# Kernel tuning notes

Measured on AMD Instinct MI355X. Metric: run time of the kernel, lower is better.

## Reference

```python
import jax, jax.numpy as jnp
import numpy as np

B, C, T = 32, 64, 8192
OUT, K = 129, 32
TWO_PI = 2.0 * np.pi
DROP_THRESH = 0.1  # squared-distance threshold for channel dropping


def setup_inputs() -> dict:
    key = jax.random.key(0)
    k1, k2, k3, k4, k5 = jax.random.split(key, 5)
    X = jax.random.normal(k1, (B, C, T), dtype=jnp.float32)
    positions = jax.random.uniform(k2, (B, C, 2), dtype=jnp.float32)
    drop_idx = jax.random.randint(k3, (B,), 0, C)
    scale = 1.0 / (K * K)
    z_real = jax.random.normal(k4, (OUT, K * K), dtype=jnp.float32) * scale
    z_imag = jax.random.normal(k5, (OUT, K * K), dtype=jnp.float32) * scale
    return {"X": X, "positions": positions, "drop_idx": drop_idx,
            "z_real": z_real, "z_imag": z_imag}


def reference(X, positions, drop_idx, z_real, z_imag):
    # frequency grid: feature index f = l_idx*K + k_idx (row-major over [l, k])
    kk = jnp.arange(1, K + 1, dtype=jnp.float32)
    coef_k = jnp.tile(kk, K)            # [K*K] varies fastest
    coef_l = jnp.repeat(kk, K)          # [K*K]

    x = positions[..., 0]               # [B, C]
    y = positions[..., 1]
    # phase: [B, C, K*K]
    phase = TWO_PI * (x[..., None] * coef_k + y[..., None] * coef_l)
    cos_mat = jnp.cos(phase)
    sin_mat = jnp.sin(phase)

    # a: [B, OUT, C]
    a = (jnp.einsum('of,bcf->boc', z_real, cos_mat)
         + jnp.einsum('of,bcf->boc', z_imag, sin_mat))

    # channel drop: remove all channels within sqdist < 0.1 of the dropped electrode
    pd = positions[jnp.arange(B), drop_idx]                 # [B, 2]
    dist = jnp.sum((positions - pd[:, None, :]) ** 2, axis=-1)  # [B, C]
    keep = dist >= DROP_THRESH                              # [B, C]

    a = jnp.where(keep[:, None, :], a, -1e9)
    attn = jax.nn.softmax(a, axis=2)                        # [B, OUT, C]
    # out: [B, OUT, T]
    return jnp.einsum('boc,bct->bot', attn, X)
```

## Files before the change

kernel.cpp:

```cpp
#include <hip/hip_runtime.h>
#include <math.h>

typedef __bf16 bf16x8 __attribute__((ext_vector_type(8)));
typedef unsigned short u16x8 __attribute__((ext_vector_type(8)));
typedef float f32x4 __attribute__((ext_vector_type(4)));

namespace {
constexpr int kB   = 32;
constexpr int kC   = 64;
constexpr int kT   = 8192;
constexpr int kOUT = 129;
constexpr int kKK  = 1024;
constexpr int kNKC = 8;
constexpr int kOP  = 144;
}

__device__ inline float sin2pi(float r) {
  float o; asm("v_sin_f32 %0, %1" : "=v"(o) : "v"(r)); return o;
}
__device__ inline float cos2pi(float r) {
  float o; asm("v_cos_f32 %0, %1" : "=v"(o) : "v"(r)); return o;
}
__device__ inline unsigned short f2bf_rne(float f) {
  unsigned int u = __builtin_bit_cast(unsigned int, f);
  return (unsigned short)((u + 0x7fffu + ((u >> 16) & 1u)) >> 16);
}
__device__ inline float bf2f(unsigned short h) {
  return __builtin_bit_cast(float, (unsigned int)h << 16);
}
__device__ inline void split8(const float* v, bf16x8& hi, bf16x8& lo) {
  u16x8 h, l;
#pragma unroll
  for (int j = 0; j < 8; ++j) {
    const unsigned short hh = f2bf_rne(v[j]);
    h[j] = hh;
    l[j] = f2bf_rne(v[j] - bf2f(hh));
  }
  hi = __builtin_bit_cast(bf16x8, h);
  lo = __builtin_bit_cast(bf16x8, l);
}
__device__ inline bf16x8 ldbf8(const unsigned short* p) {
  return __builtin_bit_cast(bf16x8, *reinterpret_cast<const u16x8*>(p));
}

__global__ __launch_bounds__(256) void sa_split_z(
    const float* __restrict__ z_real, const float* __restrict__ z_imag,
    unsigned short* __restrict__ zrh, unsigned short* __restrict__ zrl,
    unsigned short* __restrict__ zih, unsigned short* __restrict__ zil)
{
  const int i = blockIdx.x * 256 + threadIdx.x;
  if (i >= 128 * kOP * 8) return;
  const int fj = i & 7;
  const int o  = (i >> 3) % kOP;
  const int fb = i / (kOP * 8);
  const int f  = fb * 8 + fj;
  float vr = 0.f, vi = 0.f;
  if (o < kOUT) {
    vr = z_real[(size_t)o * kKK + f];
    vi = z_imag[(size_t)o * kKK + f];
  }
  unsigned short h = f2bf_rne(vr);
  zrh[i] = h; zrl[i] = f2bf_rne(vr - bf2f(h));
  h = f2bf_rne(vi);
  zih[i] = h; zil[i] = f2bf_rne(vi - bf2f(h));
}

__global__ __launch_bounds__(256) void sa_cis(
    const float* __restrict__ positions,
    unsigned short* __restrict__ csh, unsigned short* __restrict__ csl,
    unsigned short* __restrict__ snh, unsigned short* __restrict__ snl)
{
  const int i = blockIdx.x * 256 + threadIdx.x;
  const int fj = i & 7;
  const int c  = (i >> 3) & 63;
  const int fb = (i >> 9) & 127;
  const int b  = i >> 16;
  const int f  = fb * 8 + fj;
  const float2 p = reinterpret_cast<const float2*>(positions)[b * kC + c];
  const float kf = (float)((f & 31) + 1);
  const float lf = (float)((f >> 5) + 1);
  const float w = __fadd_rn(__fmul_rn(p.x, kf), __fmul_rn(p.y, lf));
  const float r = w - floorf(w);
  const float cs = cos2pi(r);
  const float sn = sin2pi(r);
  unsigned short h = f2bf_rne(cs);
  csh[i] = h; csl[i] = f2bf_rne(cs - bf2f(h));
  h = f2bf_rne(sn);
  snh[i] = h; snl[i] = f2bf_rne(sn - bf2f(h));
}

__global__ __launch_bounds__(256) void sa_phase_gemm(
    const unsigned short* __restrict__ zrh, const unsigned short* __restrict__ zrl,
    const unsigned short* __restrict__ zih, const unsigned short* __restrict__ zil,
    const unsigned short* __restrict__ csh, const unsigned short* __restrict__ csl,
    const unsigned short* __restrict__ snh, const unsigned short* __restrict__ snl,
    float* __restrict__ part)
{
  const int bid = blockIdx.x;
  const int b   = bid & 31;
  const int kc  = (bid >> 5) & 7;
  const int mh  = bid >> 8;
  const int w    = threadIdx.x >> 6;
  const int lane = threadIdx.x & 63;
  const int cg   = lane >> 4;
  const int cl   = lane & 15;
  const int c    = w * 16 + cl;

  bf16x8 BcH[4], BcL[4], BsH[4], BsL[4];
#pragma unroll
  for (int ks = 0; ks < 4; ++ks) {
    const size_t off = ((size_t)(b * 128 + kc * 16 + ks * 4 + cg) * kC + c) * 8;
    BcH[ks] = ldbf8(csh + off);
    BcL[ks] = ldbf8(csl + off);
    BsH[ks] = ldbf8(snh + off);
    BsL[ks] = ldbf8(snl + off);
  }

  const int nm  = mh ? 4 : 5;
  const int ob0 = mh * 80;

#pragma unroll
  for (int m = 0; m < 5; ++m) {
    if (m < nm) {
      const int ob = ob0 + m * 16;
      const int oa = ob + cl;
      f32x4 acc = {0.f, 0.f, 0.f, 0.f};
#pragma unroll
      for (int ks = 0; ks < 4; ++ks) {
        const size_t zo = ((size_t)(kc * 16 + ks * 4 + cg) * kOP + oa) * 8;
        const bf16x8 ArH = ldbf8(zrh + zo);
        const bf16x8 ArL = ldbf8(zrl + zo);
        const bf16x8 AiH = ldbf8(zih + zo);
        const bf16x8 AiL = ldbf8(zil + zo);
        acc = __builtin_amdgcn_mfma_f32_16x16x32_bf16(ArH, BcH[ks], acc, 0, 0, 0);
        acc = __builtin_amdgcn_mfma_f32_16x16x32_bf16(ArH, BcL[ks], acc, 0, 0, 0);
        acc = __builtin_amdgcn_mfma_f32_16x16x32_bf16(ArL, BcH[ks], acc, 0, 0, 0);
        acc = __builtin_amdgcn_mfma_f32_16x16x32_bf16(AiH, BsH[ks], acc, 0, 0, 0);
        acc = __builtin_amdgcn_mfma_f32_16x16x32_bf16(AiH, BsL[ks], acc, 0, 0, 0);
        acc = __builtin_amdgcn_mfma_f32_16x16x32_bf16(AiL, BsH[ks], acc, 0, 0, 0);
      }
#pragma unroll
      for (int r = 0; r < 4; ++r) {
        const int o = ob + cg * 4 + r;
        if (o < kOUT)
          part[(((size_t)kc * kB + b) * kOUT + o) * kC + c] = acc[r];
      }
    }
  }
}

__global__ __launch_bounds__(256) void sa_softmax(
    const float* __restrict__ part,
    const float* __restrict__ positions,
    const int*   __restrict__ drop_idx,
    unsigned short* __restrict__ a_hi,
    unsigned short* __restrict__ a_lo)
{
  const int bo = blockIdx.x * 4 + (threadIdx.x >> 6);
  if (bo >= kB * kOUT) return;
  const int b = bo / kOUT;
  const int o = bo - b * kOUT;
  const int c = threadIdx.x & 63;

  float a = 0.f;
#pragma unroll
  for (int fc = 0; fc < kNKC; ++fc)
    a += part[(((size_t)fc * kB + b) * kOUT + o) * kC + c];

  const float2 p  = reinterpret_cast<const float2*>(positions)[b * kC + c];
  const int    di = drop_idx[b];
  const float2 pd = reinterpret_cast<const float2*>(positions)[b * kC + di];
  const float dx = p.x - pd.x;
  const float dy = p.y - pd.y;
  const float d2 = __fadd_rn(__fmul_rn(dx, dx), __fmul_rn(dy, dy));
  if (d2 < 0.1f) a = -1e9f;

  float m = a;
#pragma unroll
  for (int off = 32; off; off >>= 1) m = fmaxf(m, __shfl_xor(m, off));
  const float e = expf(a - m);
  float s = e;
#pragma unroll
  for (int off = 32; off; off >>= 1) s += __shfl_xor(s, off);

  const float att = e / s;
  const unsigned short h = f2bf_rne(att);
  a_hi[(size_t)bo * kC + c] = h;
  a_lo[(size_t)bo * kC + c] = f2bf_rne(att - bf2f(h));
}

__global__ __launch_bounds__(256) void sa_apply_mfma(
    const float* __restrict__ X,
    const unsigned short* __restrict__ a_hi,
    const unsigned short* __restrict__ a_lo,
    float* __restrict__ out)
{
  __shared__ unsigned short s_a[2 * 144 * kC];

  const int b   = blockIdx.x >> 5;
  const int tc  = blockIdx.x & 31;
  const int t0  = tc * 256;
  const int tid = threadIdx.x;

  {
    char* sb = reinterpret_cast<char*>(s_a);
    for (int i = tid; i < 2 * 144 * 8; i += 256) {
      const int tile = (i >= 144 * 8) ? 1 : 0;
      const int r    = (i >> 3) - tile * 144;
      const int ch   = i & 7;
      float4 v;
      if (r < kOUT) {
        const unsigned short* src =
            (tile ? a_lo : a_hi) + ((size_t)b * kOUT + r) * kC + ch * 8;
        v = *reinterpret_cast<const float4*>(src);
      } else {
        v = make_float4(0.f, 0.f, 0.f, 0.f);
      }
      const int byte = tile * (144 * 128) + r * 128 + ((ch * 16) ^ ((r & 7) << 4));
      *reinterpret_cast<float4*>(sb + byte) = v;
    }
  }

  const int wave = tid >> 6;
  const int lane = tid & 63;
  const int cl   = lane & 15;
  const int cg   = lane >> 4;
  const int tb   = t0 + wave * 64;

  const float* Xb = X + (size_t)b * kC * kT;
  bf16x8 Xh[4][2], Xl[4][2];
#pragma unroll
  for (int n = 0; n < 4; ++n) {
    const int t = tb + n * 16 + cl;
    float xv[16];
#pragma unroll
    for (int s2 = 0; s2 < 2; ++s2)
#pragma unroll
      for (int j = 0; j < 8; ++j)
        xv[s2 * 8 + j] = Xb[(size_t)(s2 * 32 + cg * 8 + j) * kT + t];
    split8(xv,     Xh[n][0], Xl[n][0]);
    split8(xv + 8, Xh[n][1], Xl[n][1]);
  }

  __syncthreads();

  const char* sb = reinterpret_cast<const char*>(s_a);
  float* outb = out + (size_t)b * kOUT * kT;

  for (int m = 0; m < 9; ++m) {
    const int row  = m * 16 + cl;
    const int base = row * 128;
    const int sw   = (row & 7) << 4;
    const int gb   = cg * 16;

    const bf16x8 Ah0 = *reinterpret_cast<const bf16x8*>(sb + base + ((gb     ) ^ sw));
    const bf16x8 Ah1 = *reinterpret_cast<const bf16x8*>(sb + base + ((gb + 64) ^ sw));
    const bf16x8 Al0 = *reinterpret_cast<const bf16x8*>(sb + 144 * 128 + base + ((gb     ) ^ sw));
    const bf16x8 Al1 = *reinterpret_cast<const bf16x8*>(sb + 144 * 128 + base + ((gb + 64) ^ sw));

    f32x4 acc[4];
#pragma unroll
    for (int n = 0; n < 4; ++n) {
      acc[n] = f32x4{0.f, 0.f, 0.f, 0.f};
      acc[n] = __builtin_amdgcn_mfma_f32_16x16x32_bf16(Ah0, Xh[n][0], acc[n], 0, 0, 0);
      acc[n] = __builtin_amdgcn_mfma_f32_16x16x32_bf16(Ah1, Xh[n][1], acc[n], 0, 0, 0);
      acc[n] = __builtin_amdgcn_mfma_f32_16x16x32_bf16(Al0, Xh[n][0], acc[n], 0, 0, 0);
      acc[n] = __builtin_amdgcn_mfma_f32_16x16x32_bf16(Al1, Xh[n][1], acc[n], 0, 0, 0);
      acc[n] = __builtin_amdgcn_mfma_f32_16x16x32_bf16(Ah0, Xl[n][0], acc[n], 0, 0, 0);
      acc[n] = __builtin_amdgcn_mfma_f32_16x16x32_bf16(Ah1, Xl[n][1], acc[n], 0, 0, 0);
    }

#pragma unroll
    for (int n = 0; n < 4; ++n)
#pragma unroll
      for (int r = 0; r < 4; ++r) {
        const int o = m * 16 + cg * 4 + r;
        if (o < kOUT)
          outb[(size_t)o * kT + tb + n * 16 + cl] = acc[n][r];
      }
  }
}

extern "C" void kernel_launch(void* const* d_in, const int* in_sizes, int n_in,
                              void* d_out, int out_size, void* d_ws, size_t ws_size,
                              hipStream_t stream) {
  (void)in_sizes; (void)n_in; (void)out_size; (void)ws_size;
  const float* X         = (const float*)d_in[0];
  const float* positions = (const float*)d_in[1];
  const int*   drop_idx  = (const int*)d_in[2];
  const float* z_real    = (const float*)d_in[3];
  const float* z_imag    = (const float*)d_in[4];
  float* out = (float*)d_out;

  char* wsb = (char*)d_ws;
  float* part = (float*)wsb;
  unsigned short* ahi = (unsigned short*)(wsb + 8454144);
  unsigned short* alo = ahi + 264192;
  unsigned short* zrh = alo + 264192;
  unsigned short* zrl = zrh + 147456;
  unsigned short* zih = zrl + 147456;
  unsigned short* zil = zih + 147456;
  unsigned short* csh = zil + 147456;
  unsigned short* csl = csh + 2097152;
  unsigned short* snh = csl + 2097152;
  unsigned short* snl = snh + 2097152;

  sa_split_z<<<576, 256, 0, stream>>>(z_real, z_imag, zrh, zrl, zih, zil);
  sa_cis<<<8192, 256, 0, stream>>>(positions, csh, csl, snh, snl);
  sa_phase_gemm<<<kB * kNKC * 2, 256, 0, stream>>>(zrh, zrl, zih, zil,
                                                   csh, csl, snh, snl, part);
  sa_softmax<<<(kB * kOUT + 3) / 4, 256, 0, stream>>>(part, positions, drop_idx, ahi, alo);
  sa_apply_mfma<<<kB * 32, 256, 0, stream>>>(X, ahi, alo, out);
}
```

Before: 235.5 us.

## Drop LDS staging in apply kernel and spread time tiles over more blocks

The attention-apply kernel now gives each wave 16 time columns instead of 64 and launches four times as many blocks. It reads the padded bf16 hi/lo attention rows straight from global memory (through the cache) rather than staging them in swizzled shared memory behind a barrier. The softmax kernel now writes zero-padded rows up to 144, so the apply kernel needs no bounds handling on loads. Two independent accumulator chains replace the single chain per tile to expose more MFMA parallelism. The aim is better occupancy and latency hiding on this bandwidth-bound stage, at the cost of redundant attention loads per wave and a larger workspace layout.

Result: slower. 278.1 us (+18.1%).

```diff
diff --git a/kernel.cpp b/kernel.cpp
--- a/kernel.cpp
+++ b/kernel.cpp
@@ -156,11 +156,16 @@
     unsigned short* __restrict__ a_hi,
     unsigned short* __restrict__ a_lo)
 {
-  const int bo = blockIdx.x * 4 + (threadIdx.x >> 6);
-  if (bo >= kB * kOUT) return;
-  const int b = bo / kOUT;
-  const int o = bo - b * kOUT;
-  const int c = threadIdx.x & 63;
+  const int bop = blockIdx.x * 4 + (threadIdx.x >> 6);
+  const int b  = bop / kOP;
+  const int o  = bop - b * kOP;
+  const int c  = threadIdx.x & 63;
+
+  if (o >= kOUT) {
+    a_hi[(size_t)bop * kC + c] = 0;
+    a_lo[(size_t)bop * kC + c] = 0;
+    return;
+  }
 
   float a = 0.f;
 #pragma unroll
@@ -185,8 +190,8 @@
 
   const float att = e / s;
   const unsigned short h = f2bf_rne(att);
-  a_hi[(size_t)bo * kC + c] = h;
-  a_lo[(size_t)bo * kC + c] = f2bf_rne(att - bf2f(h));
+  a_hi[(size_t)bop * kC + c] = h;
+  a_lo[(size_t)bop * kC + c] = f2bf_rne(att - bf2f(h));
 }
 
 __global__ __launch_bounds__(256) void sa_apply_mfma(
@@ -195,89 +200,54 @@
     const unsigned short* __restrict__ a_lo,
     float* __restrict__ out)
 {
-  __shared__ unsigned short s_a[2 * 144 * kC];
-
-  const int b   = blockIdx.x >> 5;
-  const int tc  = blockIdx.x & 31;
-  const int t0  = tc * 256;
-  const int tid = threadIdx.x;
-
-  {
-    char* sb = reinterpret_cast<char*>(s_a);
-    for (int i = tid; i < 2 * 144 * 8; i += 256) {
-      const int tile = (i >= 144 * 8) ? 1 : 0;
-      const int r    = (i >> 3) - tile * 144;
-      const int ch   = i & 7;
-      float4 v;
-      if (r < kOUT) {
-        const unsigned short* src =
-            (tile ? a_lo : a_hi) + ((size_t)b * kOUT + r) * kC + ch * 8;
-        v = *reinterpret_cast<const float4*>(src);
-      } else {
-        v = make_float4(0.f, 0.f, 0.f, 0.f);
-      }
-      const int byte = tile * (144 * 128) + r * 128 + ((ch * 16) ^ ((r & 7) << 4));
-      *reinterpret_cast<float4*>(sb + byte) = v;
-    }
-  }
-
-  const int wave = tid >> 6;
-  const int lane = tid & 63;
+  const int b    = blockIdx.x >> 7;
+  const int tc   = blockIdx.x & 127;
+  const int wave = threadIdx.x >> 6;
+  const int lane = threadIdx.x & 63;
   const int cl   = lane & 15;
   const int cg   = lane >> 4;
-  const int tb   = t0 + wave * 64;
+  const int t    = tc * 64 + wave * 16 + cl;
 
   const float* Xb = X + (size_t)b * kC * kT;
-  bf16x8 Xh[4][2], Xl[4][2];
-#pragma unroll
-  for (int n = 0; n < 4; ++n) {
-    const int t = tb + n * 16 + cl;
-    float xv[16];
-#pragma unroll
-    for (int s2 = 0; s2 < 2; ++s2)
-#pragma unroll
-      for (int j = 0; j < 8; ++j)
-        xv[s2 * 8 + j] = Xb[(size_t)(s2 * 32 + cg * 8 + j) * kT + t];
-    split8(xv,     Xh[n][0], Xl[n][0]);
-    split8(xv + 8, Xh[n][1], Xl[n][1]);
-  }
-
-  __syncthreads();
-
-  const char* sb = reinterpret_cast<const char*>(s_a);
+  float xv[16];
+#pragma unroll
+  for (int s2 = 0; s2 < 2; ++s2)
+#pragma unroll
+    for (int j = 0; j < 8; ++j)
+      xv[s2 * 8 + j] = Xb[(size_t)(s2 * 32 + cg * 8 + j) * kT + t];
+
+  bf16x8 Xh0, Xl0, Xh1, Xl1;
+  split8(xv,     Xh0, Xl0);
+  split8(xv + 8, Xh1, Xl1);
+
+  const unsigned short* Ah = a_hi + (size_t)b * kOP * kC;
+  const unsigned short* Al = a_lo + (size_t)b * kOP * kC;
   float* outb = out + (size_t)b * kOUT * kT;
 
+#pragma unroll 3
   for (int m = 0; m < 9; ++m) {
-    const int row  = m * 16 + cl;
-    const int base = row * 128;
-    const int sw   = (row & 7) << 4;
-    const int gb   = cg * 16;
-
-    const bf16x8 Ah0 = *reinterpret_cast<const bf16x8*>(sb + base + ((gb     ) ^ sw));
-    const bf16x8 Ah1 = *reinterpret_cast<const bf16x8*>(sb + base + ((gb + 64) ^ sw));
-    const bf16x8 Al0 = *reinterpret_cast<const bf16x8*>(sb + 144 * 128 + base + ((gb     ) ^ sw));
-    const bf16x8 Al1 = *reinterpret_cast<const bf16x8*>(sb + 144 * 128 + base + ((gb + 64) ^ sw));
-
-    f32x4 acc[4];
-#pragma unroll
-    for (int n = 0; n < 4; ++n) {
-      acc[n] = f32x4{0.f, 0.f, 0.f, 0.f};
-      acc[n] = __builtin_amdgcn_mfma_f32_16x16x32_bf16(Ah0, Xh[n][0], acc[n], 0, 0, 0);
-      acc[n] = __builtin_amdgcn_mfma_f32_16x16x32_bf16(Ah1, Xh[n][1], acc[n], 0, 0, 0);
-      acc[n] = __builtin_amdgcn_mfma_f32_16x16x32_bf16(Al0, Xh[n][0], acc[n], 0, 0, 0);
-      acc[n] = __builtin_amdgcn_mfma_f32_16x16x32_bf16(Al1, Xh[n][1], acc[n], 0, 0, 0);
-      acc[n] = __builtin_amdgcn_mfma_f32_16x16x32_bf16(Ah0, Xl[n][0], acc[n], 0, 0, 0);
-      acc[n] = __builtin_amdgcn_mfma_f32_16x16x32_bf16(Ah1, Xl[n][1], acc[n], 0, 0, 0);
+    const int row = m * 16 + cl;
+    const size_t ra = (size_t)row * kC + cg * 8;
+    const bf16x8 Ah0 = ldbf8(Ah + ra);
+    const bf16x8 Ah1 = ldbf8(Ah + ra + 32);
+    const bf16x8 Al0 = ldbf8(Al + ra);
+    const bf16x8 Al1 = ldbf8(Al + ra + 32);
+
+    f32x4 p = {0.f, 0.f, 0.f, 0.f};
+    f32x4 q = {0.f, 0.f, 0.f, 0.f};
+    p = __builtin_amdgcn_mfma_f32_16x16x32_bf16(Ah0, Xh0, p, 0, 0, 0);
+    q = __builtin_amdgcn_mfma_f32_16x16x32_bf16(Ah1, Xh1, q, 0, 0, 0);
+    p = __builtin_amdgcn_mfma_f32_16x16x32_bf16(Al0, Xh0, p, 0, 0, 0);
+    q = __builtin_amdgcn_mfma_f32_16x16x32_bf16(Al1, Xh1, q, 0, 0, 0);
+    p = __builtin_amdgcn_mfma_f32_16x16x32_bf16(Ah0, Xl0, p, 0, 0, 0);
+    q = __builtin_amdgcn_mfma_f32_16x16x32_bf16(Ah1, Xl1, q, 0, 0, 0);
+
+#pragma unroll
+    for (int r = 0; r < 4; ++r) {
+      const int o = m * 16 + cg * 4 + r;
+      if (o < kOUT)
+        outb[(size_t)o * kT + t] = p[r] + q[r];
     }
-
-#pragma unroll
-    for (int n = 0; n < 4; ++n)
-#pragma unroll
-      for (int r = 0; r < 4; ++r) {
-        const int o = m * 16 + cg * 4 + r;
-        if (o < kOUT)
-          outb[(size_t)o * kT + tb + n * 16 + cl] = acc[n][r];
-      }
   }
 }
 
@@ -295,8 +265,8 @@
   char* wsb = (char*)d_ws;
   float* part = (float*)wsb;
   unsigned short* ahi = (unsigned short*)(wsb + 8454144);
-  unsigned short* alo = ahi + 264192;
-  unsigned short* zrh = alo + 264192;
+  unsigned short* alo = ahi + (size_t)kB * kOP * kC;
+  unsigned short* zrh = alo + (size_t)kB * kOP * kC;
   unsigned short* zrl = zrh + 147456;
   unsigned short* zih = zrl + 147456;
   unsigned short* zil = zih + 147456;
@@ -309,6 +279,6 @@
   sa_cis<<<8192, 256, 0, stream>>>(positions, csh, csl, snh, snl);
   sa_phase_gemm<<<kB * kNKC * 2, 256, 0, stream>>>(zrh, zrl, zih, zil,
                                                    csh, csl, snh, snl, part);
-  sa_softmax<<<(kB * kOUT + 3) / 4, 256, 0, stream>>>(part, positions, drop_idx, ahi, alo);
-  sa_apply_mfma<<<kB * 32, 256, 0, stream>>>(X, ahi, alo, out);
-}
+  sa_softmax<<<kB * kOP / 4, 256, 0, stream>>>(part, positions, drop_idx, ahi, alo);
+  sa_apply_mfma<<<kB * 128, 256, 0, stream>>>(X, ahi, alo, out);
+}
```
